# Optimization experiments

Measured on AMD Instinct MI355X. Metric: run time of the kernel, lower is better.

The kernel has to match this reference:

```python
import jax, jax.numpy as jnp
import numpy as np

N_NODES = 50000
N_EDGES = 800000
D = 128


def _gcn_conv(x, edge_index, W, b):
    """PyG GCNConv: out = D^{-1/2} (A + I) D^{-1/2} (x W) + b.

    edge_index[0] = source nodes, edge_index[1] = target nodes.
    Self-loops handled analytically instead of materializing them.
    """
    n = x.shape[0]
    src, dst = edge_index[0], edge_index[1]
    h = x @ W  # [N, out]
    # degree with self-loop: in-degree of target + 1
    deg = jax.ops.segment_sum(jnp.ones_like(dst, dtype=h.dtype), dst, num_segments=n) + 1.0
    dinv = jax.lax.rsqrt(deg)  # deg >= 1, safe
    norm = dinv[src] * dinv[dst]  # [E]
    msgs = norm[:, None] * h[src]  # [E, out]  (the big irregular-gather intermediate)
    agg = jax.ops.segment_sum(msgs, dst, num_segments=n)
    # self-loop contribution: norm = dinv[i]*dinv[i] = 1/deg
    agg = agg + h * (1.0 / deg)[:, None]
    return agg + b


def setup_inputs() -> dict:
    key = jax.random.key(0)
    k1, k2, k3, k4 = jax.random.split(key, 4)
    x = jax.random.normal(k1, (N_NODES, D), dtype=jnp.float32)
    edge_index = jax.random.randint(k2, (2, N_EDGES), 0, N_NODES, dtype=jnp.int64)
    scale = 1.0 / np.sqrt(D)
    W1 = jax.random.normal(k3, (D, D), dtype=jnp.float32) * scale
    W2 = jax.random.normal(k4, (D, D), dtype=jnp.float32) * scale
    b1 = jnp.zeros((D,), dtype=jnp.float32)
    b2 = jnp.zeros((D,), dtype=jnp.float32)
    return {"x": x, "edge_index": edge_index, "W1": W1, "b1": b1, "W2": W2, "b2": b2}


def reference(x, edge_index, W1, b1, W2, b2):
    h = _gcn_conv(x, edge_index, W1, b1)
    h = jax.nn.relu(h)  # dropout p=0.0 -> identity
    out = _gcn_conv(h, edge_index, W2, b2)
    return out
```

## Files before the change

kernel.cpp:

```cpp
#include <hip/hip_runtime.h>

#define DF 128
#define NBKT_MAX 256
#define CAP 8192

typedef unsigned int uint;
typedef unsigned short ushort;
typedef __attribute__((ext_vector_type(8))) short short8;
typedef __attribute__((ext_vector_type(4))) float f32x4;

union frag_u { uint4 u4; short8 s8; };

__device__ __forceinline__ uint f2u(float f) { return __float_as_uint(f); }
__device__ __forceinline__ ushort rne_bf16(float v) {
    uint u = __float_as_uint(v);
    u = u + 0x7FFFu + ((u >> 16) & 1u);
    return (ushort)(u >> 16);
}
__device__ __forceinline__ float bflo(uint u) { return __uint_as_float(u << 16); }
__device__ __forceinline__ float bfhi(uint u) { return __uint_as_float(u & 0xFFFF0000u); }

__global__ __launch_bounds__(256) void scatter_wprep(const int* __restrict__ src,
                                                     const int* __restrict__ dst,
                                                     int* __restrict__ ccur,
                                                     uint* __restrict__ ebuf,
                                                     int E, int NB, int SB,
                                                     const float* __restrict__ W1,
                                                     const float* __restrict__ W2,
                                                     uint4* __restrict__ Whi,
                                                     uint4* __restrict__ Wlo) {
    __shared__ int cnt[NBKT_MAX];
    __shared__ int base[NBKT_MAX];
    int t = threadIdx.x;
    if ((int)blockIdx.x < SB) {
        int e0 = blockIdx.x * 8192, e1 = min(E, e0 + 8192);
        for (int i = t; i < NB; i += 256) cnt[i] = 0;
        __syncthreads();
        for (int e = e0 + t; e < e1; e += 256) atomicAdd(&cnt[dst[e] >> 8], 1);
        __syncthreads();
        for (int i = t; i < NB; i += 256) base[i] = cnt[i] ? atomicAdd(&ccur[i], cnt[i]) : 0;
        __syncthreads();
        for (int e = e0 + t; e < e1; e += 256) {
            int d = dst[e];
            int b = d >> 8;
            int pos = atomicAdd(&base[b], 1);
            if (pos < CAP) ebuf[(size_t)b * CAP + pos] = ((uint)(d & 255) << 24) | (uint)src[e];
        }
    } else {
        int tt4 = ((int)blockIdx.x - SB) * 256 + t;
        int wsel = tt4 >> 11;
        int tt = tt4 & 2047;
        const float* W = wsel ? W2 : W1;
        int lane = tt & 63;
        int n  = ((tt >> 6) & 7) * 16 + (lane & 15);
        int k0 = (tt >> 9) * 32 + (lane >> 4) * 8;
        uint hi[4], lo[4];
#pragma unroll
        for (int p = 0; p < 4; ++p) {
            float f0 = W[(size_t)(k0 + 2 * p) * DF + n];
            float f1 = W[(size_t)(k0 + 2 * p + 1) * DF + n];
            uint u0 = f2u(f0), u1 = f2u(f1);
            hi[p] = (u1 & 0xFFFF0000u) | (u0 >> 16);
            float l0 = f0 - __uint_as_float(u0 & 0xFFFF0000u);
            float l1 = f1 - __uint_as_float(u1 & 0xFFFF0000u);
            lo[p] = (f2u(l1) & 0xFFFF0000u) | (f2u(l0) >> 16);
        }
        Whi[wsel * 2048 + tt] = make_uint4(hi[0], hi[1], hi[2], hi[3]);
        Wlo[wsel * 2048 + tt] = make_uint4(lo[0], lo[1], lo[2], lo[3]);
    }
}

__global__ __launch_bounds__(256) void bucket_sort(const uint* __restrict__ ebuf,
                                                   const int* __restrict__ ccur,
                                                   int* __restrict__ rstart,
                                                   int* __restrict__ rend,
                                                   float* __restrict__ dinv,
                                                   ushort* __restrict__ srcs,
                                                   int N) {
    __shared__ int cnt[256];
    __shared__ int sp[256];
    int t = threadIdx.x, b = blockIdx.x;
    int count = min(ccur[b], CAP);
    const uint* eb = ebuf + (size_t)b * CAP;
    cnt[t] = 0;
    __syncthreads();
    for (int j = t; j < count; j += 256) atomicAdd(&cnt[eb[j] >> 24], 1);
    __syncthreads();
    int v = cnt[t];
    sp[t] = v;
    __syncthreads();
    for (int off = 1; off < 256; off <<= 1) {
        int x = (t >= off) ? sp[t - off] : 0;
        __syncthreads();
        sp[t] += x;
        __syncthreads();
    }
    int ex = sp[t] - v;
    int node = b * 256 + t;
    if (node < N) {
        rstart[node] = b * CAP + ex;
        rend[node]   = b * CAP + ex + v;
        dinv[node] = rsqrtf((float)v + 1.0f);
    }
    sp[t] = ex;
    __syncthreads();
    for (int j = t; j < count; j += 256) {
        uint e = eb[j];
        int pos = atomicAdd(&sp[e >> 24], 1);
        srcs[(size_t)b * CAP + pos] = (ushort)(e & 0xFFFFFFu);
    }
}

__global__ __launch_bounds__(256) void gemm_f32A(const float* __restrict__ A,
                                                 const uint4* __restrict__ Bhi,
                                                 const uint4* __restrict__ Blo,
                                                 const float* __restrict__ dinv,
                                                 ushort* __restrict__ Hq, int M) {
    const int lane = threadIdx.x & 63;
    const int w = threadIdx.x >> 6;
    const int l15 = lane & 15, quad = lane >> 4;
    const int rowbase = blockIdx.x * 128 + w * 32;

    f32x4 acc[2][8];
#pragma unroll
    for (int rt = 0; rt < 2; ++rt)
#pragma unroll
        for (int ct = 0; ct < 8; ++ct) acc[rt][ct] = (f32x4){0.f, 0.f, 0.f, 0.f};

    for (int q = 0; q < 4; ++q) {
        frag_u ah[2], al[2];
#pragma unroll
        for (int rt = 0; rt < 2; ++rt) {
            int m = rowbase + rt * 16 + l15;
            if (m >= M) m = M - 1;
            const float* ap = A + (size_t)m * DF + q * 32 + quad * 8;
            float4 v0 = *(const float4*)ap;
            float4 v1 = *(const float4*)(ap + 4);
            float f[8] = {v0.x, v0.y, v0.z, v0.w, v1.x, v1.y, v1.z, v1.w};
            uint hi[4], lo[4];
#pragma unroll
            for (int p = 0; p < 4; ++p) {
                uint u0 = f2u(f[2 * p]), u1 = f2u(f[2 * p + 1]);
                hi[p] = (u1 & 0xFFFF0000u) | (u0 >> 16);
                float l0 = f[2 * p]     - __uint_as_float(u0 & 0xFFFF0000u);
                float l1 = f[2 * p + 1] - __uint_as_float(u1 & 0xFFFF0000u);
                lo[p] = (f2u(l1) & 0xFFFF0000u) | (f2u(l0) >> 16);
            }
            ah[rt].u4 = make_uint4(hi[0], hi[1], hi[2], hi[3]);
            al[rt].u4 = make_uint4(lo[0], lo[1], lo[2], lo[3]);
        }
#pragma unroll
        for (int ct = 0; ct < 8; ++ct) {
            frag_u bh, bl;
            bh.u4 = Bhi[(q * 8 + ct) * 64 + lane];
            bl.u4 = Blo[(q * 8 + ct) * 64 + lane];
#pragma unroll
            for (int rt = 0; rt < 2; ++rt) {
                acc[rt][ct] = __builtin_amdgcn_mfma_f32_16x16x32_bf16(al[rt].s8, bh.s8, acc[rt][ct], 0, 0, 0);
                acc[rt][ct] = __builtin_amdgcn_mfma_f32_16x16x32_bf16(ah[rt].s8, bl.s8, acc[rt][ct], 0, 0, 0);
                acc[rt][ct] = __builtin_amdgcn_mfma_f32_16x16x32_bf16(ah[rt].s8, bh.s8, acc[rt][ct], 0, 0, 0);
            }
        }
    }
#pragma unroll
    for (int rt = 0; rt < 2; ++rt)
#pragma unroll
        for (int reg = 0; reg < 4; ++reg) {
            int row = rowbase + rt * 16 + quad * 4 + reg;
            if (row < M) {
                float di = dinv[row];
#pragma unroll
                for (int ct = 0; ct < 8; ++ct)
                    Hq[((size_t)(ct >> 1) * M + row) * 32 + (ct & 1) * 16 + l15] =
                        rne_bf16(acc[rt][ct][reg] * di);
            }
        }
}

__global__ __launch_bounds__(256) void gemm_bf16A(const ushort* __restrict__ A,
                                                  const uint4* __restrict__ Bhi,
                                                  const uint4* __restrict__ Blo,
                                                  const float* __restrict__ dinv,
                                                  ushort* __restrict__ Hq, int M) {
    const int lane = threadIdx.x & 63;
    const int w = threadIdx.x >> 6;
    const int l15 = lane & 15, quad = lane >> 4;
    const int rowbase = blockIdx.x * 128 + w * 32;

    f32x4 acc[2][8];
#pragma unroll
    for (int rt = 0; rt < 2; ++rt)
#pragma unroll
        for (int ct = 0; ct < 8; ++ct) acc[rt][ct] = (f32x4){0.f, 0.f, 0.f, 0.f};

    for (int q = 0; q < 4; ++q) {
        frag_u a[2];
#pragma unroll
        for (int rt = 0; rt < 2; ++rt) {
            int m = rowbase + rt * 16 + l15;
            if (m >= M) m = M - 1;
            const ushort* ap = A + ((size_t)q * M + m) * 32 + quad * 8;
            a[rt].u4 = *(const uint4*)ap;
        }
#pragma unroll
        for (int ct = 0; ct < 8; ++ct) {
            frag_u bh, bl;
            bh.u4 = Bhi[(q * 8 + ct) * 64 + lane];
            bl.u4 = Blo[(q * 8 + ct) * 64 + lane];
#pragma unroll
            for (int rt = 0; rt < 2; ++rt) {
                acc[rt][ct] = __builtin_amdgcn_mfma_f32_16x16x32_bf16(a[rt].s8, bl.s8, acc[rt][ct], 0, 0, 0);
                acc[rt][ct] = __builtin_amdgcn_mfma_f32_16x16x32_bf16(a[rt].s8, bh.s8, acc[rt][ct], 0, 0, 0);
            }
        }
    }
#pragma unroll
    for (int rt = 0; rt < 2; ++rt)
#pragma unroll
        for (int reg = 0; reg < 4; ++reg) {
            int row = rowbase + rt * 16 + quad * 4 + reg;
            if (row < M) {
                float di = dinv[row];
#pragma unroll
                for (int ct = 0; ct < 8; ++ct)
                    Hq[((size_t)(ct >> 1) * M + row) * 32 + (ct & 1) * 16 + l15] =
                        rne_bf16(acc[rt][ct][reg] * di);
            }
        }
}

template<bool L1>
__global__ __launch_bounds__(256) void quarter_gather(const uint4* __restrict__ H4,
                                                      const float* __restrict__ dinv,
                                                      const int* __restrict__ rstart,
                                                      const int* __restrict__ rend,
                                                      const ushort* __restrict__ srcs,
                                                      const float* __restrict__ bias,
                                                      void* __restrict__ outv, int N) {
    int t = threadIdx.x;
    int bid = blockIdx.x;
    int sub = bid & 7;
    int q = sub >> 1;
    int n = (bid >> 3) * 128 + (sub & 1) * 64 + (t >> 2);
    if (n >= N) return;
    int l = t & 3;
    const uint4* Hq4 = H4 + (size_t)q * N * 4;

    float4 bb0 = ((const float4*)bias)[q * 8 + l * 2];
    float4 bb1 = ((const float4*)bias)[q * 8 + l * 2 + 1];

    uint4 self = Hq4[(size_t)n * 4 + l];
    float a0 = bflo(self.x), a1 = bfhi(self.x), a2 = bflo(self.y), a3 = bfhi(self.y);
    float a4 = bflo(self.z), a5 = bfhi(self.z), a6 = bflo(self.w), a7 = bfhi(self.w);

    int j = rstart[n], end = rend[n];
    for (; j + 4 <= end; j += 4) {
        int s0 = srcs[j], s1 = srcs[j + 1], s2 = srcs[j + 2], s3 = srcs[j + 3];
        uint4 v0 = Hq4[(size_t)s0 * 4 + l];
        uint4 v1 = Hq4[(size_t)s1 * 4 + l];
        uint4 v2 = Hq4[(size_t)s2 * 4 + l];
        uint4 v3 = Hq4[(size_t)s3 * 4 + l];
        a0 += (bflo(v0.x) + bflo(v1.x)) + (bflo(v2.x) + bflo(v3.x));
        a1 += (bfhi(v0.x) + bfhi(v1.x)) + (bfhi(v2.x) + bfhi(v3.x));
        a2 += (bflo(v0.y) + bflo(v1.y)) + (bflo(v2.y) + bflo(v3.y));
        a3 += (bfhi(v0.y) + bfhi(v1.y)) + (bfhi(v2.y) + bfhi(v3.y));
        a4 += (bflo(v0.z) + bflo(v1.z)) + (bflo(v2.z) + bflo(v3.z));
        a5 += (bfhi(v0.z) + bfhi(v1.z)) + (bfhi(v2.z) + bfhi(v3.z));
        a6 += (bflo(v0.w) + bflo(v1.w)) + (bflo(v2.w) + bflo(v3.w));
        a7 += (bfhi(v0.w) + bfhi(v1.w)) + (bfhi(v2.w) + bfhi(v3.w));
    }
    for (; j < end; ++j) {
        uint4 v = Hq4[(size_t)srcs[j] * 4 + l];
        a0 += bflo(v.x); a1 += bfhi(v.x); a2 += bflo(v.y); a3 += bfhi(v.y);
        a4 += bflo(v.z); a5 += bfhi(v.z); a6 += bflo(v.w); a7 += bfhi(v.w);
    }
    float di = dinv[n];
    float o0 = fmaf(a0, di, bb0.x), o1 = fmaf(a1, di, bb0.y);
    float o2 = fmaf(a2, di, bb0.z), o3 = fmaf(a3, di, bb0.w);
    float o4 = fmaf(a4, di, bb1.x), o5 = fmaf(a5, di, bb1.y);
    float o6 = fmaf(a6, di, bb1.z), o7 = fmaf(a7, di, bb1.w);
    if (L1) {
        o0 = fmaxf(o0, 0.f); o1 = fmaxf(o1, 0.f); o2 = fmaxf(o2, 0.f); o3 = fmaxf(o3, 0.f);
        o4 = fmaxf(o4, 0.f); o5 = fmaxf(o5, 0.f); o6 = fmaxf(o6, 0.f); o7 = fmaxf(o7, 0.f);
        uint4 pk;
        pk.x = (uint)rne_bf16(o0) | ((uint)rne_bf16(o1) << 16);
        pk.y = (uint)rne_bf16(o2) | ((uint)rne_bf16(o3) << 16);
        pk.z = (uint)rne_bf16(o4) | ((uint)rne_bf16(o5) << 16);
        pk.w = (uint)rne_bf16(o6) | ((uint)rne_bf16(o7) << 16);
        ((uint4*)outv)[((size_t)q * N + n) * 4 + l] = pk;
    } else {
        float4* op = (float4*)((float*)outv + (size_t)n * DF + q * 32 + l * 8);
        op[0] = make_float4(o0, o1, o2, o3);
        op[1] = make_float4(o4, o5, o6, o7);
    }
}

extern "C" void kernel_launch(void* const* d_in, const int* in_sizes, int n_in,
                              void* d_out, int out_size, void* d_ws, size_t ws_size,
                              hipStream_t stream) {
    const float* x  = (const float*)d_in[0];
    const int*   ei = (const int*)d_in[1];
    const float* W1 = (const float*)d_in[2];
    const float* b1 = (const float*)d_in[3];
    const float* W2 = (const float*)d_in[4];
    const float* b2 = (const float*)d_in[5];

    const int N = in_sizes[0] / DF;
    const int E = in_sizes[1] / 2;
    const int* src = ei;
    const int* dstp = ei + E;
    const int NB = (N + 255) >> 8;
    const int SB = (E + 8191) / 8192;

    float* out = (float*)d_out;
    char* ws = (char*)d_ws;
    size_t off = 0;
    auto carve = [&](size_t bytes) { void* p = ws + off; off += (bytes + 255) & ~(size_t)255; return p; };
    ushort* Hq     = (ushort*)carve((size_t)N * DF * sizeof(ushort));
    ushort* Z1     = (ushort*)carve((size_t)N * DF * sizeof(ushort));
    float*  dinv   = (float*)carve((size_t)N * sizeof(float));
    int*    rstart = (int*)carve((size_t)N * sizeof(int));
    int*    rend   = (int*)carve((size_t)N * sizeof(int));
    uint*   ebuf   = (uint*)carve((size_t)NB * CAP * sizeof(uint));
    ushort* srcs   = (ushort*)carve((size_t)NB * CAP * sizeof(ushort));
    int*    ccur   = (int*)carve(NBKT_MAX * sizeof(int));
    uint4*  Whi    = (uint4*)carve(2 * 2048 * sizeof(uint4));
    uint4*  Wlo    = (uint4*)carve(2 * 2048 * sizeof(uint4));

    const int gemm_b = (N + 127) / 128;
    const int gath_b = ((N + 127) / 128) * 8;

    hipMemsetAsync(ccur, 0, NBKT_MAX * sizeof(int), stream);
    scatter_wprep<<<SB + 16, 256, 0, stream>>>(src, dstp, ccur, ebuf, E, NB, SB, W1, W2, Whi, Wlo);
    bucket_sort<<<NB, 256, 0, stream>>>(ebuf, ccur, rstart, rend, dinv, srcs, N);

    gemm_f32A<<<gemm_b, 256, 0, stream>>>(x, Whi, Wlo, dinv, Hq, N);
    quarter_gather<true><<<gath_b, 256, 0, stream>>>((const uint4*)Hq, dinv, rstart, rend, srcs, b1, Z1, N);

    gemm_bf16A<<<gemm_b, 256, 0, stream>>>(Z1, Whi + 2048, Wlo + 2048, dinv, Hq, N);
    quarter_gather<false><<<gath_b, 256, 0, stream>>>((const uint4*)Hq, dinv, rstart, rend, srcs, b2, out, N);
}
```

Baseline: 208.5 us.

## Switch feature layout to column halves and gather with 8 lanes per node

```diff
diff --git a/kernel.cpp b/kernel.cpp
--- a/kernel.cpp
+++ b/kernel.cpp
@@ -34,17 +34,34 @@
     int t = threadIdx.x;
     if ((int)blockIdx.x < SB) {
         int e0 = blockIdx.x * 8192, e1 = min(E, e0 + 8192);
+        int p0 = e0 >> 1, p1 = e1 >> 1;
+        const int2* dst2 = (const int2*)dst;
+        const int2* src2 = (const int2*)src;
         for (int i = t; i < NB; i += 256) cnt[i] = 0;
         __syncthreads();
-        for (int e = e0 + t; e < e1; e += 256) atomicAdd(&cnt[dst[e] >> 8], 1);
+        for (int p = p0 + t; p < p1; p += 256) {
+            int2 d = dst2[p];
+            atomicAdd(&cnt[d.x >> 8], 1);
+            atomicAdd(&cnt[d.y >> 8], 1);
+        }
+        if (t == 0 && (e1 & 1)) atomicAdd(&cnt[dst[e1 - 1] >> 8], 1);
         __syncthreads();
         for (int i = t; i < NB; i += 256) base[i] = cnt[i] ? atomicAdd(&ccur[i], cnt[i]) : 0;
         __syncthreads();
-        for (int e = e0 + t; e < e1; e += 256) {
-            int d = dst[e];
-            int b = d >> 8;
-            int pos = atomicAdd(&base[b], 1);
-            if (pos < CAP) ebuf[(size_t)b * CAP + pos] = ((uint)(d & 255) << 24) | (uint)src[e];
+        for (int p = p0 + t; p < p1; p += 256) {
+            int2 d = dst2[p];
+            int2 s = src2[p];
+            int b0 = d.x >> 8;
+            int q0 = atomicAdd(&base[b0], 1);
+            if (q0 < CAP) ebuf[(size_t)b0 * CAP + q0] = ((uint)(d.x & 255) << 24) | (uint)s.x;
+            int b1 = d.y >> 8;
+            int q1 = atomicAdd(&base[b1], 1);
+            if (q1 < CAP) ebuf[(size_t)b1 * CAP + q1] = ((uint)(d.y & 255) << 24) | (uint)s.y;
+        }
+        if (t == 0 && (e1 & 1)) {
+            int d = dst[e1 - 1], b = d >> 8;
+            int q = atomicAdd(&base[b], 1);
+            if (q < CAP) ebuf[(size_t)b * CAP + q] = ((uint)(d & 255) << 24) | (uint)src[e1 - 1];
         }
     } else {
         int tt4 = ((int)blockIdx.x - SB) * 256 + t;
@@ -115,7 +132,7 @@
                                                  const uint4* __restrict__ Bhi,
                                                  const uint4* __restrict__ Blo,
                                                  const float* __restrict__ dinv,
-                                                 ushort* __restrict__ Hq, int M) {
+                                                 ushort* __restrict__ Hh, int M) {
     const int lane = threadIdx.x & 63;
     const int w = threadIdx.x >> 6;
     const int l15 = lane & 15, quad = lane >> 4;
@@ -171,7 +188,7 @@
                 float di = dinv[row];
 #pragma unroll
                 for (int ct = 0; ct < 8; ++ct)
-                    Hq[((size_t)(ct >> 1) * M + row) * 32 + (ct & 1) * 16 + l15] =
+                    Hh[((size_t)(ct >> 2) * M + row) * 64 + (ct & 3) * 16 + l15] =
                         rne_bf16(acc[rt][ct][reg] * di);
             }
         }
@@ -181,7 +198,7 @@
                                                   const uint4* __restrict__ Bhi,
                                                   const uint4* __restrict__ Blo,
                                                   const float* __restrict__ dinv,
-                                                  ushort* __restrict__ Hq, int M) {
+                                                  ushort* __restrict__ Hh, int M) {
     const int lane = threadIdx.x & 63;
     const int w = threadIdx.x >> 6;
     const int l15 = lane & 15, quad = lane >> 4;
@@ -199,7 +216,7 @@
         for (int rt = 0; rt < 2; ++rt) {
             int m = rowbase + rt * 16 + l15;
             if (m >= M) m = M - 1;
-            const ushort* ap = A + ((size_t)q * M + m) * 32 + quad * 8;
+            const ushort* ap = A + ((size_t)(q >> 1) * M + m) * 64 + (q & 1) * 32 + quad * 8;
             a[rt].u4 = *(const uint4*)ap;
         }
 #pragma unroll
@@ -223,54 +240,57 @@
                 float di = dinv[row];
 #pragma unroll
                 for (int ct = 0; ct < 8; ++ct)
-                    Hq[((size_t)(ct >> 1) * M + row) * 32 + (ct & 1) * 16 + l15] =
+                    Hh[((size_t)(ct >> 2) * M + row) * 64 + (ct & 3) * 16 + l15] =
                         rne_bf16(acc[rt][ct][reg] * di);
             }
         }
 }
 
 template<bool L1>
-__global__ __launch_bounds__(256) void quarter_gather(const uint4* __restrict__ H4,
-                                                      const float* __restrict__ dinv,
-                                                      const int* __restrict__ rstart,
-                                                      const int* __restrict__ rend,
-                                                      const ushort* __restrict__ srcs,
-                                                      const float* __restrict__ bias,
-                                                      void* __restrict__ outv, int N) {
+__global__ __launch_bounds__(256) void half_gather(const uint4* __restrict__ H4,
+                                                   const float* __restrict__ dinv,
+                                                   const int* __restrict__ rstart,
+                                                   const int* __restrict__ rend,
+                                                   const ushort* __restrict__ srcs,
+                                                   const float* __restrict__ bias,
+                                                   void* __restrict__ outv, int N) {
     int t = threadIdx.x;
     int bid = blockIdx.x;
     int sub = bid & 7;
-    int q = sub >> 1;
-    int n = (bid >> 3) * 128 + (sub & 1) * 64 + (t >> 2);
+    int h = sub & 1;
+    int slice = sub >> 1;
+    int n = (bid >> 3) * 128 + slice * 32 + (t >> 3);
     if (n >= N) return;
-    int l = t & 3;
-    const uint4* Hq4 = H4 + (size_t)q * N * 4;
-
-    float4 bb0 = ((const float4*)bias)[q * 8 + l * 2];
-    float4 bb1 = ((const float4*)bias)[q * 8 + l * 2 + 1];
-
-    uint4 self = Hq4[(size_t)n * 4 + l];
+    int l = t & 7;
+    const uint4* Hh = H4 + (size_t)h * N * 8;
+
+    float4 bb0 = ((const float4*)bias)[h * 16 + l * 2];
+    float4 bb1 = ((const float4*)bias)[h * 16 + l * 2 + 1];
+
+    uint4 self = Hh[(size_t)n * 8 + l];
     float a0 = bflo(self.x), a1 = bfhi(self.x), a2 = bflo(self.y), a3 = bfhi(self.y);
     float a4 = bflo(self.z), a5 = bfhi(self.z), a6 = bflo(self.w), a7 = bfhi(self.w);
 
     int j = rstart[n], end = rend[n];
-    for (; j + 4 <= end; j += 4) {
-        int s0 = srcs[j], s1 = srcs[j + 1], s2 = srcs[j + 2], s3 = srcs[j + 3];
-        uint4 v0 = Hq4[(size_t)s0 * 4 + l];
-        uint4 v1 = Hq4[(size_t)s1 * 4 + l];
-        uint4 v2 = Hq4[(size_t)s2 * 4 + l];
-        uint4 v3 = Hq4[(size_t)s3 * 4 + l];
-        a0 += (bflo(v0.x) + bflo(v1.x)) + (bflo(v2.x) + bflo(v3.x));
-        a1 += (bfhi(v0.x) + bfhi(v1.x)) + (bfhi(v2.x) + bfhi(v3.x));
-        a2 += (bflo(v0.y) + bflo(v1.y)) + (bflo(v2.y) + bflo(v3.y));
-        a3 += (bfhi(v0.y) + bfhi(v1.y)) + (bfhi(v2.y) + bfhi(v3.y));
-        a4 += (bflo(v0.z) + bflo(v1.z)) + (bflo(v2.z) + bflo(v3.z));
-        a5 += (bfhi(v0.z) + bfhi(v1.z)) + (bfhi(v2.z) + bfhi(v3.z));
-        a6 += (bflo(v0.w) + bflo(v1.w)) + (bflo(v2.w) + bflo(v3.w));
-        a7 += (bfhi(v0.w) + bfhi(v1.w)) + (bfhi(v2.w) + bfhi(v3.w));
+    while (j + 8 <= end) {
+        int sv = srcs[j + l];
+        uint4 v[8];
+#pragma unroll
+        for (int r = 0; r < 8; ++r) {
+            int s = __shfl(sv, r, 8);
+            v[r] = Hh[(size_t)s * 8 + l];
+        }
+#pragma unroll
+        for (int r = 0; r < 8; ++r) {
+            a0 += bflo(v[r].x); a1 += bfhi(v[r].x);
+            a2 += bflo(v[r].y); a3 += bfhi(v[r].y);
+            a4 += bflo(v[r].z); a5 += bfhi(v[r].z);
+            a6 += bflo(v[r].w); a7 += bfhi(v[r].w);
+        }
+        j += 8;
     }
     for (; j < end; ++j) {
-        uint4 v = Hq4[(size_t)srcs[j] * 4 + l];
+        uint4 v = Hh[(size_t)srcs[j] * 8 + l];
         a0 += bflo(v.x); a1 += bfhi(v.x); a2 += bflo(v.y); a3 += bfhi(v.y);
         a4 += bflo(v.z); a5 += bfhi(v.z); a6 += bflo(v.w); a7 += bfhi(v.w);
     }
@@ -287,9 +307,9 @@
         pk.y = (uint)rne_bf16(o2) | ((uint)rne_bf16(o3) << 16);
         pk.z = (uint)rne_bf16(o4) | ((uint)rne_bf16(o5) << 16);
         pk.w = (uint)rne_bf16(o6) | ((uint)rne_bf16(o7) << 16);
-        ((uint4*)outv)[((size_t)q * N + n) * 4 + l] = pk;
+        ((uint4*)outv)[((size_t)h * N + n) * 8 + l] = pk;
     } else {
-        float4* op = (float4*)((float*)outv + (size_t)n * DF + q * 32 + l * 8);
+        float4* op = (float4*)((float*)outv + (size_t)n * DF + h * 64 + l * 8);
         op[0] = make_float4(o0, o1, o2, o3);
         op[1] = make_float4(o4, o5, o6, o7);
     }
@@ -316,7 +336,7 @@
     char* ws = (char*)d_ws;
     size_t off = 0;
     auto carve = [&](size_t bytes) { void* p = ws + off; off += (bytes + 255) & ~(size_t)255; return p; };
-    ushort* Hq     = (ushort*)carve((size_t)N * DF * sizeof(ushort));
+    ushort* Hh     = (ushort*)carve((size_t)N * DF * sizeof(ushort));
     ushort* Z1     = (ushort*)carve((size_t)N * DF * sizeof(ushort));
     float*  dinv   = (float*)carve((size_t)N * sizeof(float));
     int*    rstart = (int*)carve((size_t)N * sizeof(int));
@@ -334,9 +354,9 @@
     scatter_wprep<<<SB + 16, 256, 0, stream>>>(src, dstp, ccur, ebuf, E, NB, SB, W1, W2, Whi, Wlo);
     bucket_sort<<<NB, 256, 0, stream>>>(ebuf, ccur, rstart, rend, dinv, srcs, N);
 
-    gemm_f32A<<<gemm_b, 256, 0, stream>>>(x, Whi, Wlo, dinv, Hq, N);
-    quarter_gather<true><<<gath_b, 256, 0, stream>>>((const uint4*)Hq, dinv, rstart, rend, srcs, b1, Z1, N);
-
-    gemm_bf16A<<<gemm_b, 256, 0, stream>>>(Z1, Whi + 2048, Wlo + 2048, dinv, Hq, N);
-    quarter_gather<false><<<gath_b, 256, 0, stream>>>((const uint4*)Hq, dinv, rstart, rend, srcs, b2, out, N);
-}
+    gemm_f32A<<<gemm_b, 256, 0, stream>>>(x, Whi, Wlo, dinv, Hh, N);
+    half_gather<true><<<gath_b, 256, 0, stream>>>((const uint4*)Hh, dinv, rstart, rend, srcs, b1, Z1, N);
+
+    gemm_bf16A<<<gemm_b, 256, 0, stream>>>(Z1, Whi + 2048, Wlo + 2048, dinv, Hh, N);
+    half_gather<false><<<gath_b, 256, 0, stream>>>((const uint4*)Hh, dinv, rstart, rend, srcs, b2, out, N);
+}
```

Result: no change. 208.5 us (+0.0%).

## Use XCD-affine work-stealing gather and vectorize edge bucketing loads

Applied to the files above, without the earlier changes.

```diff
diff --git a/kernel.cpp b/kernel.cpp
--- a/kernel.cpp
+++ b/kernel.cpp
@@ -19,6 +19,10 @@
 }
 __device__ __forceinline__ float bflo(uint u) { return __uint_as_float(u << 16); }
 __device__ __forceinline__ float bfhi(uint u) { return __uint_as_float(u & 0xFFFF0000u); }
+
+__device__ __forceinline__ int xcd_id() {
+    return (int)(__builtin_amdgcn_s_getreg((31 << 11) | 20) & 7);
+}
 
 __global__ __launch_bounds__(256) void scatter_wprep(const int* __restrict__ src,
                                                      const int* __restrict__ dst,
@@ -34,17 +38,34 @@
     int t = threadIdx.x;
     if ((int)blockIdx.x < SB) {
         int e0 = blockIdx.x * 8192, e1 = min(E, e0 + 8192);
+        int p0 = e0 >> 1, p1 = e1 >> 1;
+        const int2* dst2 = (const int2*)dst;
+        const int2* src2 = (const int2*)src;
         for (int i = t; i < NB; i += 256) cnt[i] = 0;
         __syncthreads();
-        for (int e = e0 + t; e < e1; e += 256) atomicAdd(&cnt[dst[e] >> 8], 1);
+        for (int p = p0 + t; p < p1; p += 256) {
+            int2 d = dst2[p];
+            atomicAdd(&cnt[d.x >> 8], 1);
+            atomicAdd(&cnt[d.y >> 8], 1);
+        }
+        if (t == 0 && (e1 & 1)) atomicAdd(&cnt[dst[e1 - 1] >> 8], 1);
         __syncthreads();
         for (int i = t; i < NB; i += 256) base[i] = cnt[i] ? atomicAdd(&ccur[i], cnt[i]) : 0;
         __syncthreads();
-        for (int e = e0 + t; e < e1; e += 256) {
-            int d = dst[e];
-            int b = d >> 8;
-            int pos = atomicAdd(&base[b], 1);
-            if (pos < CAP) ebuf[(size_t)b * CAP + pos] = ((uint)(d & 255) << 24) | (uint)src[e];
+        for (int p = p0 + t; p < p1; p += 256) {
+            int2 d = dst2[p];
+            int2 s = src2[p];
+            int b0 = d.x >> 8;
+            int q0 = atomicAdd(&base[b0], 1);
+            if (q0 < CAP) ebuf[(size_t)b0 * CAP + q0] = ((uint)(d.x & 255) << 24) | (uint)s.x;
+            int b1 = d.y >> 8;
+            int q1 = atomicAdd(&base[b1], 1);
+            if (q1 < CAP) ebuf[(size_t)b1 * CAP + q1] = ((uint)(d.y & 255) << 24) | (uint)s.y;
+        }
+        if (t == 0 && (e1 & 1)) {
+            int d = dst[e1 - 1], b = d >> 8;
+            int q = atomicAdd(&base[b], 1);
+            if (q < CAP) ebuf[(size_t)b * CAP + q] = ((uint)(d & 255) << 24) | (uint)src[e1 - 1];
         }
     } else {
         int tt4 = ((int)blockIdx.x - SB) * 256 + t;
@@ -230,68 +251,81 @@
 }
 
 template<bool L1>
-__global__ __launch_bounds__(256) void quarter_gather(const uint4* __restrict__ H4,
-                                                      const float* __restrict__ dinv,
-                                                      const int* __restrict__ rstart,
-                                                      const int* __restrict__ rend,
-                                                      const ushort* __restrict__ srcs,
-                                                      const float* __restrict__ bias,
-                                                      void* __restrict__ outv, int N) {
+__global__ __launch_bounds__(256) void ws_gather(const uint4* __restrict__ H4,
+                                                 const float* __restrict__ dinv,
+                                                 const int* __restrict__ rstart,
+                                                 const int* __restrict__ rend,
+                                                 const ushort* __restrict__ srcs,
+                                                 const float* __restrict__ bias,
+                                                 void* __restrict__ outv,
+                                                 int* __restrict__ wcur,
+                                                 int N, int NITEMS) {
+    __shared__ int sw;
     int t = threadIdx.x;
-    int bid = blockIdx.x;
-    int sub = bid & 7;
-    int q = sub >> 1;
-    int n = (bid >> 3) * 128 + (sub & 1) * 64 + (t >> 2);
-    if (n >= N) return;
-    int l = t & 3;
-    const uint4* Hq4 = H4 + (size_t)q * N * 4;
-
-    float4 bb0 = ((const float4*)bias)[q * 8 + l * 2];
-    float4 bb1 = ((const float4*)bias)[q * 8 + l * 2 + 1];
-
-    uint4 self = Hq4[(size_t)n * 4 + l];
-    float a0 = bflo(self.x), a1 = bfhi(self.x), a2 = bflo(self.y), a3 = bfhi(self.y);
-    float a4 = bflo(self.z), a5 = bfhi(self.z), a6 = bflo(self.w), a7 = bfhi(self.w);
-
-    int j = rstart[n], end = rend[n];
-    for (; j + 4 <= end; j += 4) {
-        int s0 = srcs[j], s1 = srcs[j + 1], s2 = srcs[j + 2], s3 = srcs[j + 3];
-        uint4 v0 = Hq4[(size_t)s0 * 4 + l];
-        uint4 v1 = Hq4[(size_t)s1 * 4 + l];
-        uint4 v2 = Hq4[(size_t)s2 * 4 + l];
-        uint4 v3 = Hq4[(size_t)s3 * 4 + l];
-        a0 += (bflo(v0.x) + bflo(v1.x)) + (bflo(v2.x) + bflo(v3.x));
-        a1 += (bfhi(v0.x) + bfhi(v1.x)) + (bfhi(v2.x) + bfhi(v3.x));
-        a2 += (bflo(v0.y) + bflo(v1.y)) + (bflo(v2.y) + bflo(v3.y));
-        a3 += (bfhi(v0.y) + bfhi(v1.y)) + (bfhi(v2.y) + bfhi(v3.y));
-        a4 += (bflo(v0.z) + bflo(v1.z)) + (bflo(v2.z) + bflo(v3.z));
-        a5 += (bfhi(v0.z) + bfhi(v1.z)) + (bfhi(v2.z) + bfhi(v3.z));
-        a6 += (bflo(v0.w) + bflo(v1.w)) + (bflo(v2.w) + bflo(v3.w));
-        a7 += (bfhi(v0.w) + bfhi(v1.w)) + (bfhi(v2.w) + bfhi(v3.w));
-    }
-    for (; j < end; ++j) {
-        uint4 v = Hq4[(size_t)srcs[j] * 4 + l];
-        a0 += bflo(v.x); a1 += bfhi(v.x); a2 += bflo(v.y); a3 += bfhi(v.y);
-        a4 += bflo(v.z); a5 += bfhi(v.z); a6 += bflo(v.w); a7 += bfhi(v.w);
-    }
-    float di = dinv[n];
-    float o0 = fmaf(a0, di, bb0.x), o1 = fmaf(a1, di, bb0.y);
-    float o2 = fmaf(a2, di, bb0.z), o3 = fmaf(a3, di, bb0.w);
-    float o4 = fmaf(a4, di, bb1.x), o5 = fmaf(a5, di, bb1.y);
-    float o6 = fmaf(a6, di, bb1.z), o7 = fmaf(a7, di, bb1.w);
-    if (L1) {
-        o0 = fmaxf(o0, 0.f); o1 = fmaxf(o1, 0.f); o2 = fmaxf(o2, 0.f); o3 = fmaxf(o3, 0.f);
-        o4 = fmaxf(o4, 0.f); o5 = fmaxf(o5, 0.f); o6 = fmaxf(o6, 0.f); o7 = fmaxf(o7, 0.f);
-        uint4 pk;
-        pk.x = (uint)rne_bf16(o0) | ((uint)rne_bf16(o1) << 16);
-        pk.y = (uint)rne_bf16(o2) | ((uint)rne_bf16(o3) << 16);
-        pk.z = (uint)rne_bf16(o4) | ((uint)rne_bf16(o5) << 16);
-        pk.w = (uint)rne_bf16(o6) | ((uint)rne_bf16(o7) << 16);
-        ((uint4*)outv)[((size_t)q * N + n) * 4 + l] = pk;
-    } else {
-        float4* op = (float4*)((float*)outv + (size_t)n * DF + q * 32 + l * 8);
-        op[0] = make_float4(o0, o1, o2, o3);
-        op[1] = make_float4(o4, o5, o6, o7);
+    int myclass = xcd_id() >> 1;
+
+    for (int c = 0; c < 4; ++c) {
+        int cls = (myclass + c) & 3;
+        const int q = cls;
+        const uint4* Hq4 = H4 + (size_t)q * N * 4;
+        while (true) {
+            __syncthreads();
+            if (t == 0) sw = atomicAdd(&wcur[cls], 1);
+            __syncthreads();
+            int w = sw;
+            if (w >= NITEMS) break;
+            int n = (w >> 2) * 256 + (w & 3) * 64 + (t >> 2);
+            if (n < N) {
+                int l = t & 3;
+                float4 bb0 = ((const float4*)bias)[q * 8 + l * 2];
+                float4 bb1 = ((const float4*)bias)[q * 8 + l * 2 + 1];
+
+                uint4 self = Hq4[(size_t)n * 4 + l];
+                float a0 = bflo(self.x), a1 = bfhi(self.x), a2 = bflo(self.y), a3 = bfhi(self.y);
+                float a4 = bflo(self.z), a5 = bfhi(self.z), a6 = bflo(self.w), a7 = bfhi(self.w);
+
+                int j = rstart[n], end = rend[n];
+                for (; j + 4 <= end; j += 4) {
+                    int s0 = srcs[j], s1 = srcs[j + 1], s2 = srcs[j + 2], s3 = srcs[j + 3];
+                    uint4 v0 = Hq4[(size_t)s0 * 4 + l];
+                    uint4 v1 = Hq4[(size_t)s1 * 4 + l];
+                    uint4 v2 = Hq4[(size_t)s2 * 4 + l];
+                    uint4 v3 = Hq4[(size_t)s3 * 4 + l];
+                    a0 += (bflo(v0.x) + bflo(v1.x)) + (bflo(v2.x) + bflo(v3.x));
+                    a1 += (bfhi(v0.x) + bfhi(v1.x)) + (bfhi(v2.x) + bfhi(v3.x));
+                    a2 += (bflo(v0.y) + bflo(v1.y)) + (bflo(v2.y) + bflo(v3.y));
+                    a3 += (bfhi(v0.y) + bfhi(v1.y)) + (bfhi(v2.y) + bfhi(v3.y));
+                    a4 += (bflo(v0.z) + bflo(v1.z)) + (bflo(v2.z) + bflo(v3.z));
+                    a5 += (bfhi(v0.z) + bfhi(v1.z)) + (bfhi(v2.z) + bfhi(v3.z));
+                    a6 += (bflo(v0.w) + bflo(v1.w)) + (bflo(v2.w) + bflo(v3.w));
+                    a7 += (bfhi(v0.w) + bfhi(v1.w)) + (bfhi(v2.w) + bfhi(v3.w));
+                }
+                for (; j < end; ++j) {
+                    uint4 v = Hq4[(size_t)srcs[j] * 4 + l];
+                    a0 += bflo(v.x); a1 += bfhi(v.x); a2 += bflo(v.y); a3 += bfhi(v.y);
+                    a4 += bflo(v.z); a5 += bfhi(v.z); a6 += bflo(v.w); a7 += bfhi(v.w);
+                }
+                float di = dinv[n];
+                float o0 = fmaf(a0, di, bb0.x), o1 = fmaf(a1, di, bb0.y);
+                float o2 = fmaf(a2, di, bb0.z), o3 = fmaf(a3, di, bb0.w);
+                float o4 = fmaf(a4, di, bb1.x), o5 = fmaf(a5, di, bb1.y);
+                float o6 = fmaf(a6, di, bb1.z), o7 = fmaf(a7, di, bb1.w);
+                if (L1) {
+                    o0 = fmaxf(o0, 0.f); o1 = fmaxf(o1, 0.f); o2 = fmaxf(o2, 0.f); o3 = fmaxf(o3, 0.f);
+                    o4 = fmaxf(o4, 0.f); o5 = fmaxf(o5, 0.f); o6 = fmaxf(o6, 0.f); o7 = fmaxf(o7, 0.f);
+                    uint4 pk;
+                    pk.x = (uint)rne_bf16(o0) | ((uint)rne_bf16(o1) << 16);
+                    pk.y = (uint)rne_bf16(o2) | ((uint)rne_bf16(o3) << 16);
+                    pk.z = (uint)rne_bf16(o4) | ((uint)rne_bf16(o5) << 16);
+                    pk.w = (uint)rne_bf16(o6) | ((uint)rne_bf16(o7) << 16);
+                    ((uint4*)outv)[((size_t)q * N + n) * 4 + l] = pk;
+                } else {
+                    float4* op = (float4*)((float*)outv + (size_t)n * DF + q * 32 + l * 8);
+                    op[0] = make_float4(o0, o1, o2, o3);
+                    op[1] = make_float4(o4, o5, o6, o7);
+                }
+            }
+        }
     }
 }
 
@@ -311,6 +345,7 @@
     const int* dstp = ei + E;
     const int NB = (N + 255) >> 8;
     const int SB = (E + 8191) / 8192;
+    const int NITEMS = NB * 4;
 
     float* out = (float*)d_out;
     char* ws = (char*)d_ws;
@@ -324,19 +359,21 @@
     uint*   ebuf   = (uint*)carve((size_t)NB * CAP * sizeof(uint));
     ushort* srcs   = (ushort*)carve((size_t)NB * CAP * sizeof(ushort));
     int*    ccur   = (int*)carve(NBKT_MAX * sizeof(int));
+    int*    wcur   = (int*)carve(8 * sizeof(int));
     uint4*  Whi    = (uint4*)carve(2 * 2048 * sizeof(uint4));
     uint4*  Wlo    = (uint4*)carve(2 * 2048 * sizeof(uint4));
 
     const int gemm_b = (N + 127) / 128;
-    const int gath_b = ((N + 127) / 128) * 8;
-
-    hipMemsetAsync(ccur, 0, NBKT_MAX * sizeof(int), stream);
+    const int gath_b = NITEMS * 4;
+
+    hipMemsetAsync(ccur, 0, NBKT_MAX * sizeof(int) + 256, stream);
+
     scatter_wprep<<<SB + 16, 256, 0, stream>>>(src, dstp, ccur, ebuf, E, NB, SB, W1, W2, Whi, Wlo);
     bucket_sort<<<NB, 256, 0, stream>>>(ebuf, ccur, rstart, rend, dinv, srcs, N);
 
     gemm_f32A<<<gemm_b, 256, 0, stream>>>(x, Whi, Wlo, dinv, Hq, N);
-    quarter_gather<true><<<gath_b, 256, 0, stream>>>((const uint4*)Hq, dinv, rstart, rend, srcs, b1, Z1, N);
+    ws_gather<true><<<gath_b, 256, 0, stream>>>((const uint4*)Hq, dinv, rstart, rend, srcs, b1, Z1, wcur, N, NITEMS);
 
     gemm_bf16A<<<gemm_b, 256, 0, stream>>>(Z1, Whi + 2048, Wlo + 2048, dinv, Hq, N);
-    quarter_gather<false><<<gath_b, 256, 0, stream>>>((const uint4*)Hq, dinv, rstart, rend, srcs, b2, out, N);
-}
+    ws_gather<false><<<gath_b, 256, 0, stream>>>((const uint4*)Hq, dinv, rstart, rend, srcs, b2, out, wcur + 4, N, NITEMS);
+}
```

New measurement: 525.2 us. +151.9%, slower.
